# Optimization experiments

Measured on AMD Instinct MI355X. Metric: run time of the kernel, lower is better.

The kernel has to match this reference:

```python
import jax, jax.numpy as jnp
import numpy as np

B, H, L, N = 8, 128, 4096, 64
EPS = 1e-7
LOG_DT_MIN, LOG_DT_MAX = np.log(0.001), np.log(0.1)


def setup_inputs() -> dict:
    key = jax.random.key(0)
    k_u, k_lre, k_w, k_step = jax.random.split(key, 4)
    u = jax.random.normal(k_u, (B, H, L), dtype=jnp.float32)
    # HiPPO-style diagonal init: Re(Lambda) < 0 for stability, Im(Lambda) = pi*n
    Lambda_re = -0.5 * jnp.ones((H, N), jnp.float32) \
        - 0.1 * jax.random.uniform(k_lre, (H, N), dtype=jnp.float32)
    Lambda_im = jnp.broadcast_to(jnp.pi * jnp.arange(N, dtype=jnp.float32), (H, N))
    # W stored as (real, imag) pairs, stddev sqrt(0.5) per the module's initializer
    W_ri = (0.5 ** 0.5) * jax.random.normal(k_w, (H, N, 2), dtype=jnp.float32)
    D = jnp.ones((H,), jnp.float32)
    # log_step ~ U[log(1e-3), log(1e-1)] per log_step_initializer
    log_step = jax.random.uniform(k_step, (H,), dtype=jnp.float32) \
        * (LOG_DT_MAX - LOG_DT_MIN) + LOG_DT_MIN
    return {"u": u, "Lambda_re": Lambda_re, "Lambda_im": Lambda_im,
            "W_ri": W_ri, "D": D, "log_step": log_step}


def _dss_kernel(W, Lambda, step, Lseq):
    # P[h,n,l] = step_h * Lambda_hn * l
    pos = jnp.arange(Lseq, dtype=jnp.float32)
    P = (step[:, None] * Lambda)[..., None] * pos          # [H,N,L] complex64
    # complex softmax over l, stabilized by the entry with largest real part
    idx = jnp.argmax(P.real, axis=-1)[..., None]           # [H,N,1]
    e = jnp.exp(P - jnp.take_along_axis(P, idx, axis=-1))
    s = jnp.sum(e, axis=-1, keepdims=True)
    S = e * (jnp.conj(s) / (s * jnp.conj(s) + EPS))        # e / s, eps-regularized
    return jnp.einsum('hn,hnl->hl', W / Lambda, S).real    # [H,L]


def reference(u, Lambda_re, Lambda_im, W_ri, D, log_step):
    Lambda = Lambda_re + 1j * Lambda_im                    # [H,N]
    W = W_ri[..., 0] + 1j * W_ri[..., 1]                   # [H,N]
    step = jnp.exp(log_step)                               # [H]
    Lseq = u.shape[-1]
    K = _dss_kernel(W, Lambda, step, Lseq)                 # [H,L]
    # FFT-based causal convolution, zero-padded to 2L
    n = 2 * Lseq
    uf = jnp.fft.rfft(u, n=n, axis=-1)                     # [B,H,L+1]
    Kf = jnp.fft.rfft(K, n=n, axis=-1)                     # [H,L+1]
    y = jnp.fft.irfft(uf * Kf[None], n=n, axis=-1)[..., :Lseq]
    return y + D[None, :, None] * u
```

## Files before the change

kernel.cpp:

```cpp
#include <hip/hip_runtime.h>
#include <math.h>

#define H_  128
#define N_  64
#define L_  4096
#define B_  8
#define LC  128
#define NCH 32

typedef _Float16 f16;
typedef _Float16 half8 __attribute__((ext_vector_type(8)));
typedef _Float16 f16x4 __attribute__((ext_vector_type(4)));
typedef _Float16 f16x2 __attribute__((ext_vector_type(2)));
typedef float    floatx4 __attribute__((ext_vector_type(4)));

#define WS_T 0
#define WS_G ((size_t)H_*LC*LC*2)
#define WS_M ((size_t)2*H_*LC*LC*2)
#define WS_Q ((size_t)3*H_*LC*LC*2)

__global__ __launch_bounds__(256)
void dss_prep(const float* __restrict__ Lre, const float* __restrict__ Lim,
              const float* __restrict__ Wri, const float* __restrict__ Dv,
              const float* __restrict__ lstep, char* __restrict__ ws)
{
    __shared__ float s_rre[N_], s_rim[N_], s_cre[N_], s_cim[N_];
    __shared__ float sRT[N_][130];
    __shared__ float sK[LC];
    const int h = blockIdx.x;
    const int t = threadIdx.x;
    f16*   Tg = (f16*)(ws + WS_T) + (size_t)h*LC*LC;
    f16*   Gg = (f16*)(ws + WS_G) + (size_t)h*LC*LC;
    f16*   Mg = (f16*)(ws + WS_M) + (size_t)h*LC*LC;
    float* qg = (float*)(ws + WS_Q) + (size_t)h*N_*2;

    if (t < N_) {
        const int n = t;
        const float stepf = expf(lstep[h]);
        const float a  = stepf * Lre[h*N_ + n];
        const float bp = stepf * Lim[h*N_ + n];
        const double ad = (double)a, bd = (double)bp;
        const double em = exp(ad);
        const double rre = em * cos(bd), rim = em * sin(bd);
        const double eL = exp(ad * (double)L_);
        const double rLre = eL * cos(bd * (double)L_), rLim = eL * sin(bd * (double)L_);
        const double nre = 1.0 - rLre, nim = -rLim;
        const double dre = 1.0 - rre,  dim = -rim;
        const double dm  = dre*dre + dim*dim;
        const double sre = (nre*dre + nim*dim) / dm;
        const double sim = (nim*dre - nre*dim) / dm;
        const double wre = (double)Wri[(h*N_ + n)*2 + 0];
        const double wim = (double)Wri[(h*N_ + n)*2 + 1];
        const double lre = (double)Lre[h*N_ + n], lim = (double)Lim[h*N_ + n];
        const double lm  = lre*lre + lim*lim;
        const double wor = (wre*lre + wim*lim) / lm;
        const double woi = (wim*lre - wre*lim) / lm;
        const double sm  = sre*sre + sim*sim + 1e-7;
        const double cre = (wor*sre + woi*sim) / sm;
        const double cim = (woi*sre - wor*sim) / sm;
        const double eC = exp(ad * (double)LC);
        s_rre[n] = (float)rre;  s_rim[n] = (float)rim;
        s_cre[n] = (float)cre;  s_cim[n] = (float)cim;
        qg[2*n]   = (float)(eC * cos(bd * (double)LC));
        qg[2*n+1] = (float)(eC * sin(bd * (double)LC));
    }
    __syncthreads();

    if (t < N_) {
        const float rr = s_rre[t], ri = s_rim[t];
        float wr = s_cre[t], wi = s_cim[t];
        for (int j = 0; j < LC; ++j) {
            sRT[t][j] = wr;
            const float nr2 = wr*rr - wi*ri, ni2 = wr*ri + wi*rr;
            wr = nr2; wi = ni2;
        }
    }
    __syncthreads();
    if (t < LC) {
        float acc = 0.f;
        for (int n = 0; n < N_; ++n) acc += sRT[n][t];
        if (t == 0) acc += Dv[h];
        sK[t] = acc;
    }
    __syncthreads();
    for (int e = t; e < LC*LC; e += 256) {
        const int i = e >> 7, j = e & 127;
        Tg[e] = (f16)((i >= j) ? sK[i-j] : 0.f);
    }
    if (t < N_) {
        const float rr = s_rre[t], ri = s_rim[t];
        {
            float wr = 1.f, wi = 0.f;
            for (int k = LC-1; k >= 0; --k) {
                Gg[(2*t)*LC + k]   = (f16)wr;
                Gg[(2*t+1)*LC + k] = (f16)wi;
                const float nr2 = wr*rr - wi*ri, ni2 = wr*ri + wi*rr;
                wr = nr2; wi = ni2;
            }
        }
        {
            float mr = (s_cre[t]*rr - s_cim[t]*ri) * 16.f;
            float mi = (s_cre[t]*ri + s_cim[t]*rr) * 16.f;
            for (int j = 0; j < LC; ++j) {
                Mg[j*LC + 2*t]   = (f16)mr;
                Mg[j*LC + 2*t+1] = (f16)(-mi);
                const float nr2 = mr*rr - mi*ri, ni2 = mr*ri + mi*rr;
                mr = nr2; mi = ni2;
            }
        }
    }
}

__global__ __launch_bounds__(256, 4)
void dss_main(const float* __restrict__ u, const char* __restrict__ ws,
              float* __restrict__ out)
{
    __shared__ f16   sU[NCH][132];
    __shared__ float sE[NCH][130];
    __shared__ f16   sC[NCH][132];

    const int t  = threadIdx.x;
    const int bh = blockIdx.x;
    const int h  = bh & (H_-1);
    const f16* Tg = (const f16*)(ws + WS_T) + (size_t)h*LC*LC;
    const f16* Gg = (const f16*)(ws + WS_G) + (size_t)h*LC*LC;
    const f16* Mg = (const f16*)(ws + WS_M) + (size_t)h*LC*LC;
    const float* qg = (const float*)(ws + WS_Q) + (size_t)h*N_*2;

    {
        const float4* up = reinterpret_cast<const float4*>(u + (size_t)bh * L_);
        #pragma unroll
        for (int i = 0; i < L_/4/256; ++i) {
            const int e4 = t + i*256;
            const float4 v = up[e4];
            const int row = e4 >> 5, c4 = (e4 & 31) * 4;
            f16x4 pv = { (f16)v.x, (f16)v.y, (f16)v.z, (f16)v.w };
            *reinterpret_cast<f16x4*>(&sU[row][c4]) = pv;
        }
    }
    __syncthreads();

    const int w  = t >> 6;
    const int l  = t & 63;
    const int lr = l & 15;
    const int lg = l >> 4;

    floatx4 accA[2][2] = {};
    floatx4 accB[2][2] = {};

    #pragma unroll
    for (int ks = 0; ks < 4; ++ks) {
        const int ko = ks*32 + lg*8;
        const half8 a0 = *reinterpret_cast<const half8*>(&sU[lr     ][ko]);
        const half8 a1 = *reinterpret_cast<const half8*>(&sU[16 + lr][ko]);
        #pragma unroll
        for (int nt = 0; nt < 2; ++nt) {
            const int ncol = (2*w + nt)*16 + lr;
            const half8 bT = *reinterpret_cast<const half8*>(&Tg[ncol*LC + ko]);
            const half8 bG = *reinterpret_cast<const half8*>(&Gg[ncol*LC + ko]);
            accA[0][nt] = __builtin_amdgcn_mfma_f32_16x16x32_f16(a0, bT, accA[0][nt], 0, 0, 0);
            accA[1][nt] = __builtin_amdgcn_mfma_f32_16x16x32_f16(a1, bT, accA[1][nt], 0, 0, 0);
            accB[0][nt] = __builtin_amdgcn_mfma_f32_16x16x32_f16(a0, bG, accB[0][nt], 0, 0, 0);
            accB[1][nt] = __builtin_amdgcn_mfma_f32_16x16x32_f16(a1, bG, accB[1][nt], 0, 0, 0);
        }
    }
    #pragma unroll
    for (int mt = 0; mt < 2; ++mt)
        #pragma unroll
        for (int nt = 0; nt < 2; ++nt)
            #pragma unroll
            for (int j = 0; j < 4; ++j)
                sE[mt*16 + lg*4 + j][(2*w + nt)*16 + lr] = accB[mt][nt][j];
    __syncthreads();

    if (w == 0) {
        const float qre = qg[2*l], qim = qg[2*l+1];
        float cr = 0.f, ci = 0.f;
        #pragma unroll
        for (int k = 0; k < NCH; ++k) {
            const float er = sE[k][2*l], ei = sE[k][2*l+1];
            *reinterpret_cast<f16x2*>(&sC[k][2*l]) =
                (f16x2){ (f16)(cr * 0.0625f), (f16)(ci * 0.0625f) };
            const float ncr = fmaf(qre, cr, fmaf(-qim, ci, er));
            const float nci = fmaf(qre, ci, fmaf( qim, cr, ei));
            cr = ncr; ci = nci;
        }
    }
    __syncthreads();

    #pragma unroll
    for (int ks = 0; ks < 4; ++ks) {
        const int ko = ks*32 + lg*8;
        const half8 a0 = *reinterpret_cast<const half8*>(&sC[lr     ][ko]);
        const half8 a1 = *reinterpret_cast<const half8*>(&sC[16 + lr][ko]);
        #pragma unroll
        for (int nt = 0; nt < 2; ++nt) {
            const int ncol = (2*w + nt)*16 + lr;
            const half8 bM = *reinterpret_cast<const half8*>(&Mg[ncol*LC + ko]);
            accA[0][nt] = __builtin_amdgcn_mfma_f32_16x16x32_f16(a0, bM, accA[0][nt], 0, 0, 0);
            accA[1][nt] = __builtin_amdgcn_mfma_f32_16x16x32_f16(a1, bM, accA[1][nt], 0, 0, 0);
        }
    }

    float* op = out + (size_t)bh * L_;
    #pragma unroll
    for (int mt = 0; mt < 2; ++mt)
        #pragma unroll
        for (int nt = 0; nt < 2; ++nt) {
            const int pos = (2*w + nt)*16 + lr;
            #pragma unroll
            for (int j = 0; j < 4; ++j) {
                const int chunk = mt*16 + lg*4 + j;
                op[chunk*LC + pos] = accA[mt][nt][j];
            }
        }
}

extern "C" void kernel_launch(void* const* d_in, const int* in_sizes, int n_in,
                              void* d_out, int out_size, void* d_ws, size_t ws_size,
                              hipStream_t stream) {
    const float* u  = (const float*)d_in[0];
    const float* lr = (const float*)d_in[1];
    const float* li = (const float*)d_in[2];
    const float* w  = (const float*)d_in[3];
    const float* dv = (const float*)d_in[4];
    const float* ls = (const float*)d_in[5];
    float* out = (float*)d_out;
    char* ws = (char*)d_ws;
    dss_prep<<<dim3(H_), dim3(256), 0, stream>>>(lr, li, w, dv, ls, ws);
    dss_main<<<dim3(B_*H_), dim3(256), 0, stream>>>(u, ws, out);
}
```

Before: 105.3 us.

## Parallelize prep across 3x blocks with closed-form powers; stage output through LDS

The prep kernel is split into three block groups (T, G, M matrices) per head. Sequential complex power recurrences run by 64 threads are replaced with direct exp/sincos evaluation, so all 256 threads work and writes are vectorized as half8. The main kernel now stages results in LDS and writes coalesced float4 stores instead of scattered scalar stores. The trade-off is that each prep block recomputes the per-mode constants in double, and direct float exp/sincos may differ numerically from the recurrence.

```diff
diff --git a/kernel.cpp b/kernel.cpp
--- a/kernel.cpp
+++ b/kernel.cpp
@@ -19,94 +19,129 @@
 #define WS_M ((size_t)2*H_*LC*LC*2)
 #define WS_Q ((size_t)3*H_*LC*LC*2)
 
+__device__ __forceinline__ void dss_consts(int h, int n,
+    const float* __restrict__ Lre, const float* __restrict__ Lim,
+    const float* __restrict__ Wri, const float* __restrict__ lstep,
+    float& af, float& bf, float& crf, float& cif, float& qrf, float& qif)
+{
+    const float stepf = expf(lstep[h]);
+    const float a  = stepf * Lre[h*N_ + n];
+    const float bp = stepf * Lim[h*N_ + n];
+    const double ad = (double)a, bd = (double)bp;
+    const double em = exp(ad);
+    const double rre = em * cos(bd), rim = em * sin(bd);
+    const double eL = exp(ad * (double)L_);
+    const double rLre = eL * cos(bd * (double)L_), rLim = eL * sin(bd * (double)L_);
+    const double nre = 1.0 - rLre, nim = -rLim;
+    const double dre = 1.0 - rre,  dim = -rim;
+    const double dm  = dre*dre + dim*dim;
+    const double sre = (nre*dre + nim*dim) / dm;
+    const double sim = (nim*dre - nre*dim) / dm;
+    const double wre = (double)Wri[(h*N_ + n)*2 + 0];
+    const double wim = (double)Wri[(h*N_ + n)*2 + 1];
+    const double lre = (double)Lre[h*N_ + n], lim = (double)Lim[h*N_ + n];
+    const double lm  = lre*lre + lim*lim;
+    const double wor = (wre*lre + wim*lim) / lm;
+    const double woi = (wim*lre - wre*lim) / lm;
+    const double sm  = sre*sre + sim*sim + 1e-7;
+    const double eC  = exp(ad * (double)LC);
+    af = a; bf = bp;
+    crf = (float)((wor*sre + woi*sim) / sm);
+    cif = (float)((woi*sre - wor*sim) / sm);
+    qrf = (float)(eC * cos(bd * (double)LC));
+    qif = (float)(eC * sin(bd * (double)LC));
+}
+
 __global__ __launch_bounds__(256)
 void dss_prep(const float* __restrict__ Lre, const float* __restrict__ Lim,
               const float* __restrict__ Wri, const float* __restrict__ Dv,
               const float* __restrict__ lstep, char* __restrict__ ws)
 {
-    __shared__ float s_rre[N_], s_rim[N_], s_cre[N_], s_cim[N_];
-    __shared__ float sRT[N_][130];
-    __shared__ float sK[LC];
+    __shared__ float s_a[N_], s_b[N_], s_cr[N_], s_ci[N_];
+    __shared__ float sKp[2][128];
+    __shared__ float sK[128];
     const int h = blockIdx.x;
+    const int which = blockIdx.y;
     const int t = threadIdx.x;
-    f16*   Tg = (f16*)(ws + WS_T) + (size_t)h*LC*LC;
-    f16*   Gg = (f16*)(ws + WS_G) + (size_t)h*LC*LC;
-    f16*   Mg = (f16*)(ws + WS_M) + (size_t)h*LC*LC;
-    float* qg = (float*)(ws + WS_Q) + (size_t)h*N_*2;
 
     if (t < N_) {
-        const int n = t;
-        const float stepf = expf(lstep[h]);
-        const float a  = stepf * Lre[h*N_ + n];
-        const float bp = stepf * Lim[h*N_ + n];
-        const double ad = (double)a, bd = (double)bp;
-        const double em = exp(ad);
-        const double rre = em * cos(bd), rim = em * sin(bd);
-        const double eL = exp(ad * (double)L_);
-        const double rLre = eL * cos(bd * (double)L_), rLim = eL * sin(bd * (double)L_);
-        const double nre = 1.0 - rLre, nim = -rLim;
-        const double dre = 1.0 - rre,  dim = -rim;
-        const double dm  = dre*dre + dim*dim;
-        const double sre = (nre*dre + nim*dim) / dm;
-        const double sim = (nim*dre - nre*dim) / dm;
-        const double wre = (double)Wri[(h*N_ + n)*2 + 0];
-        const double wim = (double)Wri[(h*N_ + n)*2 + 1];
-        const double lre = (double)Lre[h*N_ + n], lim = (double)Lim[h*N_ + n];
-        const double lm  = lre*lre + lim*lim;
-        const double wor = (wre*lre + wim*lim) / lm;
-        const double woi = (wim*lre - wre*lim) / lm;
-        const double sm  = sre*sre + sim*sim + 1e-7;
-        const double cre = (wor*sre + woi*sim) / sm;
-        const double cim = (woi*sre - wor*sim) / sm;
-        const double eC = exp(ad * (double)LC);
-        s_rre[n] = (float)rre;  s_rim[n] = (float)rim;
-        s_cre[n] = (float)cre;  s_cim[n] = (float)cim;
-        qg[2*n]   = (float)(eC * cos(bd * (double)LC));
-        qg[2*n+1] = (float)(eC * sin(bd * (double)LC));
-    }
-    __syncthreads();
-
-    if (t < N_) {
-        const float rr = s_rre[t], ri = s_rim[t];
-        float wr = s_cre[t], wi = s_cim[t];
-        for (int j = 0; j < LC; ++j) {
-            sRT[t][j] = wr;
-            const float nr2 = wr*rr - wi*ri, ni2 = wr*ri + wi*rr;
-            wr = nr2; wi = ni2;
-        }
-    }
-    __syncthreads();
-    if (t < LC) {
+        float a, b, cr, ci, qr, qi;
+        dss_consts(h, t, Lre, Lim, Wri, lstep, a, b, cr, ci, qr, qi);
+        s_a[t] = a; s_b[t] = b; s_cr[t] = cr; s_ci[t] = ci;
+        if (which == 0) {
+            float* qg = (float*)(ws + WS_Q) + (size_t)h*N_*2;
+            qg[2*t] = qr; qg[2*t+1] = qi;
+        }
+    }
+    __syncthreads();
+
+    if (which == 0) {
+        const int tt = t & 127, hf = t >> 7;
         float acc = 0.f;
-        for (int n = 0; n < N_; ++n) acc += sRT[n][t];
-        if (t == 0) acc += Dv[h];
-        sK[t] = acc;
-    }
-    __syncthreads();
-    for (int e = t; e < LC*LC; e += 256) {
-        const int i = e >> 7, j = e & 127;
-        Tg[e] = (f16)((i >= j) ? sK[i-j] : 0.f);
-    }
-    if (t < N_) {
-        const float rr = s_rre[t], ri = s_rim[t];
-        {
-            float wr = 1.f, wi = 0.f;
-            for (int k = LC-1; k >= 0; --k) {
-                Gg[(2*t)*LC + k]   = (f16)wr;
-                Gg[(2*t+1)*LC + k] = (f16)wi;
-                const float nr2 = wr*rr - wi*ri, ni2 = wr*ri + wi*rr;
-                wr = nr2; wi = ni2;
+        #pragma unroll
+        for (int m = 0; m < 32; ++m) {
+            const int n = hf*32 + m;
+            const float ex = expf(s_a[n] * (float)tt);
+            float sn, cs; sincosf(s_b[n] * (float)tt, &sn, &cs);
+            acc = fmaf(ex, s_cr[n]*cs - s_ci[n]*sn, acc);
+        }
+        sKp[hf][tt] = acc;
+        __syncthreads();
+        if (t < 128) {
+            float kv = sKp[0][t] + sKp[1][t];
+            if (t == 0) kv += Dv[h];
+            sK[t] = kv;
+        }
+        __syncthreads();
+        f16* Tg = (f16*)(ws + WS_T) + (size_t)h*LC*LC;
+        #pragma unroll
+        for (int i = 0; i < 8; ++i) {
+            const int e8 = t + i*256;
+            const int row = e8 >> 4, c0 = (e8 & 15) * 8;
+            half8 pv;
+            #pragma unroll
+            for (int j = 0; j < 8; ++j) {
+                const int col = c0 + j;
+                pv[j] = (f16)((row >= col) ? sK[row - col] : 0.f);
             }
-        }
-        {
-            float mr = (s_cre[t]*rr - s_cim[t]*ri) * 16.f;
-            float mi = (s_cre[t]*ri + s_cim[t]*rr) * 16.f;
-            for (int j = 0; j < LC; ++j) {
-                Mg[j*LC + 2*t]   = (f16)mr;
-                Mg[j*LC + 2*t+1] = (f16)(-mi);
-                const float nr2 = mr*rr - mi*ri, ni2 = mr*ri + mi*rr;
-                mr = nr2; mi = ni2;
+            *reinterpret_cast<half8*>(&Tg[row*LC + c0]) = pv;
+        }
+    } else if (which == 1) {
+        f16* Gg = (f16*)(ws + WS_G) + (size_t)h*LC*LC;
+        #pragma unroll
+        for (int i = 0; i < 8; ++i) {
+            const int e8 = t + i*256;
+            const int row = e8 >> 4, c0 = (e8 & 15) * 8;
+            const int m = row >> 1, im = row & 1;
+            const float a = s_a[m], b = s_b[m];
+            half8 pv;
+            #pragma unroll
+            for (int j = 0; j < 8; ++j) {
+                const float p = (float)(127 - (c0 + j));
+                const float ex = expf(a * p);
+                float sn, cs; sincosf(b * p, &sn, &cs);
+                pv[j] = (f16)(im ? ex*sn : ex*cs);
             }
+            *reinterpret_cast<half8*>(&Gg[row*LC + c0]) = pv;
+        }
+    } else {
+        f16* Mg = (f16*)(ws + WS_M) + (size_t)h*LC*LC;
+        #pragma unroll
+        for (int i = 0; i < 8; ++i) {
+            const int e8 = t + i*256;
+            const int row = e8 >> 4, c0 = (e8 & 15) * 8;
+            const float p = (float)(row + 1);
+            half8 pv;
+            #pragma unroll
+            for (int mm = 0; mm < 4; ++mm) {
+                const int m = (c0 >> 1) + mm;
+                const float ex = expf(s_a[m] * p);
+                float sn, cs; sincosf(s_b[m] * p, &sn, &cs);
+                const float pr = ex*cs, pi = ex*sn;
+                pv[2*mm]   = (f16)( 16.f * (s_cr[m]*pr - s_ci[m]*pi));
+                pv[2*mm+1] = (f16)(-16.f * (s_cr[m]*pi + s_ci[m]*pr));
+            }
+            *reinterpret_cast<half8*>(&Mg[row*LC + c0]) = pv;
         }
     }
 }
@@ -116,7 +151,7 @@
               float* __restrict__ out)
 {
     __shared__ f16   sU[NCH][132];
-    __shared__ float sE[NCH][130];
+    __shared__ float sE[NCH][132];
     __shared__ f16   sC[NCH][132];
 
     const int t  = threadIdx.x;
@@ -202,18 +237,23 @@
         }
     }
 
-    float* op = out + (size_t)bh * L_;
     #pragma unroll
     for (int mt = 0; mt < 2; ++mt)
         #pragma unroll
-        for (int nt = 0; nt < 2; ++nt) {
-            const int pos = (2*w + nt)*16 + lr;
-            #pragma unroll
-            for (int j = 0; j < 4; ++j) {
-                const int chunk = mt*16 + lg*4 + j;
-                op[chunk*LC + pos] = accA[mt][nt][j];
-            }
-        }
+        for (int nt = 0; nt < 2; ++nt)
+            #pragma unroll
+            for (int j = 0; j < 4; ++j)
+                sE[mt*16 + lg*4 + j][(2*w + nt)*16 + lr] = accA[mt][nt][j];
+    __syncthreads();
+    {
+        float4* op = reinterpret_cast<float4*>(out + (size_t)bh * L_);
+        #pragma unroll
+        for (int i = 0; i < L_/4/256; ++i) {
+            const int e4 = t + i*256;
+            const int row = e4 >> 5, c4 = (e4 & 31) * 4;
+            op[e4] = *reinterpret_cast<const float4*>(&sE[row][c4]);
+        }
+    }
 }
 
 extern "C" void kernel_launch(void* const* d_in, const int* in_sizes, int n_in,
@@ -227,6 +267,6 @@
     const float* ls = (const float*)d_in[5];
     float* out = (float*)d_out;
     char* ws = (char*)d_ws;
-    dss_prep<<<dim3(H_), dim3(256), 0, stream>>>(lr, li, w, dv, ls, ws);
+    dss_prep<<<dim3(H_, 3), dim3(256), 0, stream>>>(lr, li, w, dv, ls, ws);
     dss_main<<<dim3(B_*H_), dim3(256), 0, stream>>>(u, ws, out);
 }
```

Result: no change. 105.6 us (+0.3%).
